# Kernel tuning notes

Hardware: AMD Instinct MI355X
Metric: run time of the kernel (lower is better)

The kernel has to match this reference:

```python
import jax, jax.numpy as jnp
import numpy as np

N, IN_F, E, EDGE_F, H, C = 50000, 128, 800000, 32, 4, 32
NEG_SLOPE = 0.2
EPS = 1e-16


def setup_inputs() -> dict:
    key = jax.random.key(0)
    ks = jax.random.split(key, 10)
    s = lambda *sh: 1.0 / np.sqrt(sh[-1])
    return {
        "node_features": jax.random.normal(ks[0], (N, IN_F), jnp.float32),
        "edge_features": jax.random.normal(ks[1], (E, EDGE_F), jnp.float32),
        "edge_index": jax.random.randint(ks[2], (2, E), 0, N, jnp.int32),
        # GATConv params
        "W_gat": jax.random.normal(ks[3], (H * C, IN_F), jnp.float32) * s(IN_F),
        "att_src": jax.random.normal(ks[4], (H, C), jnp.float32) * s(C),
        "att_dst": jax.random.normal(ks[5], (H, C), jnp.float32) * s(C),
        "att_edge": jax.random.normal(ks[6], (H, C), jnp.float32) * s(C),
        "bias": jnp.zeros((H * C,), jnp.float32),
        # edge_linear and skip_connection weights
        "W_edge": jax.random.normal(ks[7], (H * C, EDGE_F), jnp.float32) * s(EDGE_F),
        "W_skip": jax.random.normal(ks[8], (H * C, IN_F), jnp.float32) * s(IN_F),
    }


def reference(node_features, edge_features, edge_index, W_gat, att_src, att_dst,
              att_edge, bias, W_edge, W_skip):
    src, dst = edge_index[0], edge_index[1]
    # edge_linear + view(-1, H, C)
    e_attr = (edge_features @ W_edge.T).reshape(E, H, C)
    # GATConv: per-head linear transform of nodes -> [N, H, C]
    x = (node_features @ W_gat.T).reshape(N, H, C)
    # attention logits: a_src.x_i + a_dst.x_j + a_edge.e  -> [E, H]
    a_src = jnp.einsum('nhc,hc->nh', x, att_src)
    a_dst = jnp.einsum('nhc,hc->nh', x, att_dst)
    a_edge = jnp.einsum('ehc,hc->eh', e_attr, att_edge)
    alpha = jax.nn.leaky_relu(a_src[src] + a_dst[dst] + a_edge, NEG_SLOPE)
    # segment softmax over incoming edges of each destination node
    m = jax.ops.segment_max(alpha, dst, num_segments=N)  # [N, H]
    m = jnp.where(jnp.isfinite(m), m, 0.0)
    ex = jnp.exp(alpha - m[dst])
    denom = jax.ops.segment_sum(ex, dst, num_segments=N)  # [N, H]
    attn = ex / (denom[dst] + EPS)  # [E, H]
    # message = alpha * x_src ; scatter-add to destination
    msg = x[src] * attn[:, :, None]  # [E, H, C]
    out = jax.ops.segment_sum(msg, dst, num_segments=N)  # [N, H, C]
    out = out.reshape(N, H * C) + bias  # concat=True
    # skip connection + ELU activation
    out = out + node_features @ W_skip.T
    return jax.nn.elu(out)
```

## Files before the change

kernel.cpp:

```cpp
#include <hip/hip_runtime.h>
#include <hip/hip_bf16.h>

constexpr int N_NODES = 50000;
constexpr int IN_F    = 128;
constexpr long E_EDGES = 800000;
constexpr int EDGE_F  = 32;
constexpr int H_HEADS = 4;
constexpr int C_CH    = 32;
constexpr int HC      = 128;
constexpr float NEG_SLOPE = 0.2f;
constexpr float EPS = 1e-16f;
constexpr int NB_SCAN = (N_NODES + 255) / 256;
constexpr int NB_HIST = (int)((E_EDGES + 255) / 256);
constexpr float SM_SHIFT = 12.0f;

typedef __attribute__((ext_vector_type(8))) short bf16x8;
typedef __attribute__((ext_vector_type(4))) float f32x4;

__device__ __forceinline__ unsigned short f2b(float f) {
    __hip_bfloat16 h = __float2bfloat16(f);
    return *reinterpret_cast<unsigned short*>(&h);
}
__device__ __forceinline__ float b2f_lo(unsigned v) { return __uint_as_float(v << 16); }
__device__ __forceinline__ float b2f_hi(unsigned v) { return __uint_as_float(v & 0xffff0000u); }

__global__ __launch_bounds__(256) void zero_counts_kernel(int* __restrict__ counts)
{
    int i = blockIdx.x * 256 + threadIdx.x;
    if (i < N_NODES) counts[i] = 0;
}

__global__ __launch_bounds__(256) void prep_kernel(
    const float* __restrict__ Wg, const float* __restrict__ Ws,
    unsigned short* __restrict__ wcat, const float* __restrict__ We,
    const float* __restrict__ att_edge, float* __restrict__ weff,
    const int* __restrict__ dst, int* __restrict__ counts,
    int* __restrict__ rank)
{
    const int b = blockIdx.x, t = threadIdx.x;
    if (b < 32) {
        int i = (b * 256 + t) * 4;
        const float* srcp = (i < 16384) ? (Wg + i) : (Ws + i - 16384);
        float4 v = *(const float4*)srcp;
        ushort4 o;
        o.x = f2b(v.x); o.y = f2b(v.y); o.z = f2b(v.z); o.w = f2b(v.w);
        *(ushort4*)&wcat[i] = o;
    } else if (b == 32) {
        if (t < 128) {
            int h = t >> 5, f = t & 31;
            float acc = 0.f;
#pragma unroll
            for (int c = 0; c < C_CH; ++c)
                acc = fmaf(We[(h * C_CH + c) * EDGE_F + f], att_edge[h * C_CH + c], acc);
            weff[t] = acc;
        }
    } else {
        long e = (long)(b - 33) * 256 + t;
        if (e < E_EDGES) rank[e] = atomicAdd(&counts[dst[e]], 1);
    }
}

__global__ __launch_bounds__(256) void mfma_gemm_kernel(
    const float* __restrict__ nf, const unsigned short* __restrict__ wcat,
    const float* __restrict__ bias, unsigned short* __restrict__ xb,
    float* __restrict__ out)
{
    const int t  = threadIdx.x;
    const int w  = t >> 6;
    const int l  = t & 63;
    const int lr = l & 15;
    const int lk = l >> 4;
    const int n0 = blockIdx.x * 64;

    bf16x8 bfr[4][4];
#pragma unroll
    for (int nfr = 0; nfr < 4; ++nfr)
#pragma unroll
        for (int ks = 0; ks < 4; ++ks)
            bfr[nfr][ks] = *(const bf16x8*)&wcat[(w * 64 + nfr * 16 + lr) * 128 + ks * 32 + lk * 8];

    f32x4 acc[4][4];
#pragma unroll
    for (int mf = 0; mf < 4; ++mf)
#pragma unroll
        for (int nfr = 0; nfr < 4; ++nfr)
            acc[mf][nfr] = (f32x4){0.f, 0.f, 0.f, 0.f};

#pragma unroll
    for (int ks = 0; ks < 4; ++ks) {
        bf16x8 afr[4];
#pragma unroll
        for (int mf = 0; mf < 4; ++mf) {
            int row = n0 + mf * 16 + lr;
            row = row < N_NODES ? row : N_NODES - 1;
            const float* ap = nf + (size_t)row * IN_F + ks * 32 + lk * 8;
            float4 a0 = *(const float4*)ap;
            float4 a1 = *(const float4*)(ap + 4);
            bf16x8 f;
            f[0] = (short)f2b(a0.x); f[1] = (short)f2b(a0.y);
            f[2] = (short)f2b(a0.z); f[3] = (short)f2b(a0.w);
            f[4] = (short)f2b(a1.x); f[5] = (short)f2b(a1.y);
            f[6] = (short)f2b(a1.z); f[7] = (short)f2b(a1.w);
            afr[mf] = f;
        }
#pragma unroll
        for (int mf = 0; mf < 4; ++mf)
#pragma unroll
            for (int nfr = 0; nfr < 4; ++nfr)
                acc[mf][nfr] = __builtin_amdgcn_mfma_f32_16x16x32_bf16(
                    afr[mf], bfr[nfr][ks], acc[mf][nfr], 0, 0, 0);
    }

#pragma unroll
    for (int nfr = 0; nfr < 4; ++nfr) {
        const int gc = w * 64 + nfr * 16 + lr;
        if (gc < HC) {
#pragma unroll
            for (int mf = 0; mf < 4; ++mf)
#pragma unroll
                for (int r = 0; r < 4; ++r) {
                    int m = n0 + mf * 16 + lk * 4 + r;
                    if (m < N_NODES) xb[(size_t)m * HC + gc] = f2b(acc[mf][nfr][r]);
                }
        } else {
            const float bv = bias[gc - HC];
#pragma unroll
            for (int mf = 0; mf < 4; ++mf)
#pragma unroll
                for (int r = 0; r < 4; ++r) {
                    int m = n0 + mf * 16 + lk * 4 + r;
                    if (m < N_NODES) out[(size_t)m * HC + gc - HC] = acc[mf][nfr][r] + bv;
                }
        }
    }
}

__global__ __launch_bounds__(256) void a_kernel(
    const unsigned int* __restrict__ xb32, const float* __restrict__ att_src,
    const float* __restrict__ att_dst, float* __restrict__ asrc,
    float* __restrict__ adst)
{
    const int wave = threadIdx.x >> 6, lane = threadIdx.x & 63;
    const int n = blockIdx.x * 4 + wave;
    if (n >= N_NODES) return;
    unsigned v = xb32[(size_t)n * 64 + lane];
    float x0 = b2f_lo(v), x1 = b2f_hi(v);
    float2 as = ((const float2*)att_src)[lane];
    float2 ad = ((const float2*)att_dst)[lane];
    float ps = x0 * as.x + x1 * as.y;
    float pd = x0 * ad.x + x1 * ad.y;
#pragma unroll
    for (int off = 1; off < 16; off <<= 1) {
        ps += __shfl_xor(ps, off);
        pd += __shfl_xor(pd, off);
    }
    if ((lane & 15) == 0) {
        asrc[(size_t)n * H_HEADS + (lane >> 4)] = ps;
        adst[(size_t)n * H_HEADS + (lane >> 4)] = pd;
    }
}

__global__ __launch_bounds__(256) void scan1_kernel(const int* __restrict__ counts,
                                                    int* __restrict__ row_ptr,
                                                    int* __restrict__ blocksum)
{
    __shared__ int s[256];
    int t = threadIdx.x;
    int i = blockIdx.x * 256 + t;
    int v = (i < N_NODES) ? counts[i] : 0;
    s[t] = v;
    __syncthreads();
#pragma unroll
    for (int off = 1; off < 256; off <<= 1) {
        int u = (t >= off) ? s[t - off] : 0;
        __syncthreads();
        s[t] += u;
        __syncthreads();
    }
    if (i < N_NODES) row_ptr[i] = s[t] - v;
    if (t == 255) blocksum[blockIdx.x] = s[255];
}

__global__ __launch_bounds__(256) void scan2_kernel(int* __restrict__ blocksum)
{
    __shared__ int s[256];
    int t = threadIdx.x;
    int v = (t < NB_SCAN) ? blocksum[t] : 0;
    s[t] = v;
    __syncthreads();
#pragma unroll
    for (int off = 1; off < 256; off <<= 1) {
        int u = (t >= off) ? s[t - off] : 0;
        __syncthreads();
        s[t] += u;
        __syncthreads();
    }
    blocksum[t] = s[t] - v;
}

__global__ __launch_bounds__(256) void scan3_kernel(int* __restrict__ row_ptr,
                                                    const int* __restrict__ blocksum)
{
    int i = blockIdx.x * 256 + threadIdx.x;
    if (i < N_NODES) row_ptr[i] = row_ptr[i] + blocksum[blockIdx.x];
    if (i == 0) row_ptr[N_NODES] = (int)E_EDGES;
}

__global__ __launch_bounds__(256) void edge_logits_kernel(
    const float* __restrict__ ef, const int* __restrict__ src,
    const int* __restrict__ dst, const float* __restrict__ weff,
    const float* __restrict__ asrc, const float* __restrict__ adst,
    const int* __restrict__ row_ptr, const int* __restrict__ rank,
    unsigned int* __restrict__ rec)
{
    __shared__ float ef_lds[64][36];
    __shared__ float wf[4][36];
    const int t = threadIdx.x;
    const long e0 = (long)blockIdx.x * 64;

#pragma unroll
    for (int j = 0; j < 2; ++j) {
        int i4 = t + j * 256;
        int el = i4 >> 3, f4 = i4 & 7;
        long e = e0 + el;
        float4 v = (e < E_EDGES) ? ((const float4*)ef)[e * 8 + f4]
                                 : make_float4(0.f, 0.f, 0.f, 0.f);
        ef_lds[el][f4 * 4 + 0] = v.x; ef_lds[el][f4 * 4 + 1] = v.y;
        ef_lds[el][f4 * 4 + 2] = v.z; ef_lds[el][f4 * 4 + 3] = v.w;
    }
    if (t < 128) wf[t >> 5][t & 31] = weff[t];
    __syncthreads();

    const int el = t >> 2, h = t & 3;
    const long e = e0 + el;
    if (e < E_EDGES) {
        float acc = 0.f;
#pragma unroll
        for (int f4 = 0; f4 < 8; ++f4) {
            float4 a = *(const float4*)&ef_lds[el][f4 * 4];
            float4 b = *(const float4*)&wf[h][f4 * 4];
            acc = fmaf(a.x, b.x, acc); acc = fmaf(a.y, b.y, acc);
            acc = fmaf(a.z, b.z, acc); acc = fmaf(a.w, b.w, acc);
        }
        int s = src[e], d = dst[e];
        float logit = asrc[(size_t)s * H_HEADS + h] + adst[(size_t)d * H_HEADS + h] + acc;
        float al = logit > 0.f ? logit : NEG_SLOPE * logit;
        int pos = row_ptr[d] + rank[e];
        unsigned w = (__float_as_uint(al) & 0xFFFFFF00u)
                   | ((unsigned)(s >> (8 * h)) & 0xFFu);
        rec[(size_t)pos * 4 + h] = w;
    }
}

__device__ __forceinline__ void accum8(float* acc, uint4 v, float e) {
    acc[0] = fmaf(b2f_lo(v.x), e, acc[0]);
    acc[1] = fmaf(b2f_hi(v.x), e, acc[1]);
    acc[2] = fmaf(b2f_lo(v.y), e, acc[2]);
    acc[3] = fmaf(b2f_hi(v.y), e, acc[3]);
    acc[4] = fmaf(b2f_lo(v.z), e, acc[4]);
    acc[5] = fmaf(b2f_hi(v.z), e, acc[5]);
    acc[6] = fmaf(b2f_lo(v.w), e, acc[6]);
    acc[7] = fmaf(b2f_hi(v.w), e, acc[7]);
}

__device__ __forceinline__ int rec_src(uint4 r) {
    return (int)((r.x & 0xFFu) | ((r.y & 0xFFu) << 8));
}
__device__ __forceinline__ float rec_alpha(uint4 r, int h) {
    unsigned w = h == 0 ? r.x : h == 1 ? r.y : h == 2 ? r.z : r.w;
    return __uint_as_float(w & 0xFFFFFF00u);
}

__global__ __launch_bounds__(256) void aggregate_kernel(
    const int* __restrict__ row_ptr, const uint4* __restrict__ rec4,
    const uint4* __restrict__ xb4, float* __restrict__ out)
{
    const int wave = threadIdx.x >> 6;
    const int lane = threadIdx.x & 63;
    const int d = blockIdx.x * 4 + wave;
    if (d >= N_NODES) return;
    const int beg = row_ptr[d], end = row_ptr[d + 1];
    const int q  = lane >> 4;
    const int cg = lane & 15;
    const int h  = cg >> 2;

    float acc[8] = {0.f, 0.f, 0.f, 0.f, 0.f, 0.f, 0.f, 0.f};
    float dsum = 0.f;

    int i = beg;
    for (; i + 8 <= end; i += 8) {
        int i0 = i + q, i1 = i + 4 + q;
        uint4 r0 = rec4[i0];
        uint4 r1 = rec4[i1];
        int s0 = rec_src(r0);
        int s1 = rec_src(r1);
        float a0 = rec_alpha(r0, h);
        float a1 = rec_alpha(r1, h);
        uint4 v0 = xb4[(size_t)s0 * 16 + cg];
        uint4 v1 = xb4[(size_t)s1 * 16 + cg];
        float e0 = __expf(a0 - SM_SHIFT);
        float e1 = __expf(a1 - SM_SHIFT);
        dsum += e0 + e1;
        accum8(acc, v0, e0);
        accum8(acc, v1, e1);
    }
    for (; i < end; i += 4) {
        int idx = i + q;
        bool val = idx < end;
        int ii = val ? idx : end - 1;
        uint4 r = rec4[ii];
        int s = rec_src(r);
        float a = rec_alpha(r, h);
        uint4 v = xb4[(size_t)s * 16 + cg];
        float e = val ? __expf(a - SM_SHIFT) : 0.f;
        dsum += e;
        accum8(acc, v, e);
    }

#pragma unroll
    for (int off = 16; off <= 32; off <<= 1) {
        dsum += __shfl_xor(dsum, off);
#pragma unroll
        for (int k = 0; k < 8; ++k) acc[k] += __shfl_xor(acc[k], off);
    }
    const float inv = 1.f / (dsum + EPS);

    if (q == 0) {
        float* op = out + (size_t)d * HC + cg * 8;
        float4 o0 = *(const float4*)op;
        float4 o1 = *(const float4*)(op + 4);
        o0.x += acc[0] * inv; o0.y += acc[1] * inv;
        o0.z += acc[2] * inv; o0.w += acc[3] * inv;
        o1.x += acc[4] * inv; o1.y += acc[5] * inv;
        o1.z += acc[6] * inv; o1.w += acc[7] * inv;
        o0.x = o0.x > 0.f ? o0.x : expf(o0.x) - 1.f;
        o0.y = o0.y > 0.f ? o0.y : expf(o0.y) - 1.f;
        o0.z = o0.z > 0.f ? o0.z : expf(o0.z) - 1.f;
        o0.w = o0.w > 0.f ? o0.w : expf(o0.w) - 1.f;
        o1.x = o1.x > 0.f ? o1.x : expf(o1.x) - 1.f;
        o1.y = o1.y > 0.f ? o1.y : expf(o1.y) - 1.f;
        o1.z = o1.z > 0.f ? o1.z : expf(o1.z) - 1.f;
        o1.w = o1.w > 0.f ? o1.w : expf(o1.w) - 1.f;
        *(float4*)op = o0;
        *(float4*)(op + 4) = o1;
    }
}

extern "C" void kernel_launch(void* const* d_in, const int* in_sizes, int n_in,
                              void* d_out, int out_size, void* d_ws, size_t ws_size,
                              hipStream_t stream)
{
    const float* nf       = (const float*)d_in[0];
    const float* ef       = (const float*)d_in[1];
    const int*   ei       = (const int*)d_in[2];
    const float* Wg       = (const float*)d_in[3];
    const float* att_src  = (const float*)d_in[4];
    const float* att_dst  = (const float*)d_in[5];
    const float* att_edge = (const float*)d_in[6];
    const float* bias     = (const float*)d_in[7];
    const float* We       = (const float*)d_in[8];
    const float* Ws       = (const float*)d_in[9];
    float* out = (float*)d_out;

    const int* src = ei;
    const int* dst = ei + E_EDGES;

    unsigned int* rec   = (unsigned int*)d_ws;
    unsigned short* xb  = (unsigned short*)(rec + 4 * E_EDGES);
    unsigned short* wcat= xb + (size_t)N_NODES * HC;
    float* asrc         = (float*)(wcat + 256 * 128);
    float* adst         = asrc + (size_t)N_NODES * H_HEADS;
    float* weff         = adst + (size_t)N_NODES * H_HEADS;
    int*   counts       = (int*)(weff + 128);
    int*   row_ptr      = counts + N_NODES;
    int*   blocksum     = row_ptr + N_NODES + 1;
    int*   rank         = blocksum + 256;

    zero_counts_kernel<<<NB_SCAN, 256, 0, stream>>>(counts);
    prep_kernel<<<33 + NB_HIST, 256, 0, stream>>>(
        Wg, Ws, wcat, We, att_edge, weff, dst, counts, rank);
    mfma_gemm_kernel<<<(N_NODES + 63) / 64, 256, 0, stream>>>(
        nf, wcat, bias, xb, out);
    a_kernel<<<(N_NODES + 3) / 4, 256, 0, stream>>>(
        (const unsigned int*)xb, att_src, att_dst, asrc, adst);
    scan1_kernel<<<NB_SCAN, 256, 0, stream>>>(counts, row_ptr, blocksum);
    scan2_kernel<<<1, 256, 0, stream>>>(blocksum);
    scan3_kernel<<<NB_SCAN, 256, 0, stream>>>(row_ptr, blocksum);
    edge_logits_kernel<<<(int)(E_EDGES / 64), 256, 0, stream>>>(
        ef, src, dst, weff, asrc, adst, row_ptr, rank, rec);
    aggregate_kernel<<<(N_NODES + 3) / 4, 256, 0, stream>>>(
        row_ptr, (const uint4*)rec, (const uint4*)xb, out);
}
```

Baseline: 175.4 us.

## Process one edge per thread in edge logits and batch histogram atomics

The edge logits kernel now gives each thread a whole edge, computing all four heads. Each thread loads the 32 edge features directly as float4s instead of staging them through LDS. It also reads asrc/adst as one float4 each and writes the packed 4-head record as a single uint4, which cuts redundant src/dst/rank/row_ptr loads and scattered 4-byte stores. The histogram part of prep now handles four edges per thread with int4 loads and stores. The risk is more registers per thread and uncoalesced per-thread 128-byte feature reads. The edge logits kernel also drops its bounds check, which relies on E being divisible by 256.

```diff
diff --git a/kernel.cpp b/kernel.cpp
--- a/kernel.cpp
+++ b/kernel.cpp
@@ -11,7 +11,8 @@
 constexpr float NEG_SLOPE = 0.2f;
 constexpr float EPS = 1e-16f;
 constexpr int NB_SCAN = (N_NODES + 255) / 256;
-constexpr int NB_HIST = (int)((E_EDGES + 255) / 256);
+constexpr int NB_EL   = (int)(E_EDGES / 256);
+constexpr int NB_HIST4 = (int)((E_EDGES + 1023) / 1024);
 constexpr float SM_SHIFT = 12.0f;
 
 typedef __attribute__((ext_vector_type(8))) short bf16x8;
@@ -55,8 +56,19 @@
             weff[t] = acc;
         }
     } else {
-        long e = (long)(b - 33) * 256 + t;
-        if (e < E_EDGES) rank[e] = atomicAdd(&counts[dst[e]], 1);
+        long e0 = (long)(b - 33) * 1024 + t * 4;
+        if (e0 + 3 < E_EDGES) {
+            int4 d4 = *(const int4*)(dst + e0);
+            int4 r4;
+            r4.x = atomicAdd(&counts[d4.x], 1);
+            r4.y = atomicAdd(&counts[d4.y], 1);
+            r4.z = atomicAdd(&counts[d4.z], 1);
+            r4.w = atomicAdd(&counts[d4.w], 1);
+            *(int4*)(rank + e0) = r4;
+        } else {
+            for (long e = e0; e < E_EDGES; ++e)
+                rank[e] = atomicAdd(&counts[dst[e]], 1);
+        }
     }
 }
 
@@ -211,45 +223,62 @@
     const int* __restrict__ dst, const float* __restrict__ weff,
     const float* __restrict__ asrc, const float* __restrict__ adst,
     const int* __restrict__ row_ptr, const int* __restrict__ rank,
-    unsigned int* __restrict__ rec)
-{
-    __shared__ float ef_lds[64][36];
-    __shared__ float wf[4][36];
+    uint4* __restrict__ rec4)
+{
+    __shared__ float wf[128];
     const int t = threadIdx.x;
-    const long e0 = (long)blockIdx.x * 64;
-
-#pragma unroll
-    for (int j = 0; j < 2; ++j) {
-        int i4 = t + j * 256;
-        int el = i4 >> 3, f4 = i4 & 7;
-        long e = e0 + el;
-        float4 v = (e < E_EDGES) ? ((const float4*)ef)[e * 8 + f4]
-                                 : make_float4(0.f, 0.f, 0.f, 0.f);
-        ef_lds[el][f4 * 4 + 0] = v.x; ef_lds[el][f4 * 4 + 1] = v.y;
-        ef_lds[el][f4 * 4 + 2] = v.z; ef_lds[el][f4 * 4 + 3] = v.w;
-    }
-    if (t < 128) wf[t >> 5][t & 31] = weff[t];
+    if (t < 128) wf[t] = weff[t];
     __syncthreads();
 
-    const int el = t >> 2, h = t & 3;
-    const long e = e0 + el;
-    if (e < E_EDGES) {
+    const long e = (long)blockIdx.x * 256 + t;
+
+    const int s  = src[e];
+    const int d  = dst[e];
+    const int rk = rank[e];
+    const float4* efp = (const float4*)(ef + (size_t)e * EDGE_F);
+    float4 q0 = efp[0], q1 = efp[1], q2 = efp[2], q3 = efp[3];
+    float4 q4 = efp[4], q5 = efp[5], q6 = efp[6], q7 = efp[7];
+
+    float4 as4 = ((const float4*)asrc)[s];
+    float4 ad4 = ((const float4*)adst)[d];
+    const int pos = row_ptr[d] + rk;
+
+    uint4 r;
+    unsigned* rw = (unsigned*)&r;
+    float base[4] = {as4.x + ad4.x, as4.y + ad4.y, as4.z + ad4.z, as4.w + ad4.w};
+#pragma unroll
+    for (int h = 0; h < 4; ++h) {
+        const float4 w0 = *(const float4*)&wf[h * 32 + 0];
+        const float4 w1 = *(const float4*)&wf[h * 32 + 4];
+        const float4 w2 = *(const float4*)&wf[h * 32 + 8];
+        const float4 w3 = *(const float4*)&wf[h * 32 + 12];
+        const float4 w4 = *(const float4*)&wf[h * 32 + 16];
+        const float4 w5 = *(const float4*)&wf[h * 32 + 20];
+        const float4 w6 = *(const float4*)&wf[h * 32 + 24];
+        const float4 w7 = *(const float4*)&wf[h * 32 + 28];
         float acc = 0.f;
-#pragma unroll
-        for (int f4 = 0; f4 < 8; ++f4) {
-            float4 a = *(const float4*)&ef_lds[el][f4 * 4];
-            float4 b = *(const float4*)&wf[h][f4 * 4];
-            acc = fmaf(a.x, b.x, acc); acc = fmaf(a.y, b.y, acc);
-            acc = fmaf(a.z, b.z, acc); acc = fmaf(a.w, b.w, acc);
-        }
-        int s = src[e], d = dst[e];
-        float logit = asrc[(size_t)s * H_HEADS + h] + adst[(size_t)d * H_HEADS + h] + acc;
+        acc = fmaf(q0.x, w0.x, acc); acc = fmaf(q0.y, w0.y, acc);
+        acc = fmaf(q0.z, w0.z, acc); acc = fmaf(q0.w, w0.w, acc);
+        acc = fmaf(q1.x, w1.x, acc); acc = fmaf(q1.y, w1.y, acc);
+        acc = fmaf(q1.z, w1.z, acc); acc = fmaf(q1.w, w1.w, acc);
+        acc = fmaf(q2.x, w2.x, acc); acc = fmaf(q2.y, w2.y, acc);
+        acc = fmaf(q2.z, w2.z, acc); acc = fmaf(q2.w, w2.w, acc);
+        acc = fmaf(q3.x, w3.x, acc); acc = fmaf(q3.y, w3.y, acc);
+        acc = fmaf(q3.z, w3.z, acc); acc = fmaf(q3.w, w3.w, acc);
+        acc = fmaf(q4.x, w4.x, acc); acc = fmaf(q4.y, w4.y, acc);
+        acc = fmaf(q4.z, w4.z, acc); acc = fmaf(q4.w, w4.w, acc);
+        acc = fmaf(q5.x, w5.x, acc); acc = fmaf(q5.y, w5.y, acc);
+        acc = fmaf(q5.z, w5.z, acc); acc = fmaf(q5.w, w5.w, acc);
+        acc = fmaf(q6.x, w6.x, acc); acc = fmaf(q6.y, w6.y, acc);
+        acc = fmaf(q6.z, w6.z, acc); acc = fmaf(q6.w, w6.w, acc);
+        acc = fmaf(q7.x, w7.x, acc); acc = fmaf(q7.y, w7.y, acc);
+        acc = fmaf(q7.z, w7.z, acc); acc = fmaf(q7.w, w7.w, acc);
+        float logit = base[h] + acc;
         float al = logit > 0.f ? logit : NEG_SLOPE * logit;
-        int pos = row_ptr[d] + rank[e];
-        unsigned w = (__float_as_uint(al) & 0xFFFFFF00u)
-                   | ((unsigned)(s >> (8 * h)) & 0xFFu);
-        rec[(size_t)pos * 4 + h] = w;
-    }
+        rw[h] = (__float_as_uint(al) & 0xFFFFFF00u)
+              | ((unsigned)(s >> (8 * h)) & 0xFFu);
+    }
+    rec4[pos] = r;
 }
 
 __device__ __forceinline__ void accum8(float* acc, uint4 v, float e) {
@@ -377,7 +406,7 @@
     int*   rank         = blocksum + 256;
 
     zero_counts_kernel<<<NB_SCAN, 256, 0, stream>>>(counts);
-    prep_kernel<<<33 + NB_HIST, 256, 0, stream>>>(
+    prep_kernel<<<33 + NB_HIST4, 256, 0, stream>>>(
         Wg, Ws, wcat, We, att_edge, weff, dst, counts, rank);
     mfma_gemm_kernel<<<(N_NODES + 63) / 64, 256, 0, stream>>>(
         nf, wcat, bias, xb, out);
@@ -386,8 +415,8 @@
     scan1_kernel<<<NB_SCAN, 256, 0, stream>>>(counts, row_ptr, blocksum);
     scan2_kernel<<<1, 256, 0, stream>>>(blocksum);
     scan3_kernel<<<NB_SCAN, 256, 0, stream>>>(row_ptr, blocksum);
-    edge_logits_kernel<<<(int)(E_EDGES / 64), 256, 0, stream>>>(
-        ef, src, dst, weff, asrc, adst, row_ptr, rank, rec);
+    edge_logits_kernel<<<NB_EL, 256, 0, stream>>>(
+        ef, src, dst, weff, asrc, adst, row_ptr, rank, (uint4*)rec);
     aggregate_kernel<<<(N_NODES + 3) / 4, 256, 0, stream>>>(
         row_ptr, (const uint4*)rec, (const uint4*)xb, out);
 }
```

Result: slower. 191.1 us (+8.9%).

## Precompute edge logits in histogram kernel and vectorize edge record scatter

Applied to the files above, without the earlier changes.

The per-edge edge-feature dot product against the folded attention weights moves into a new prep kernel. That kernel runs alongside the vectorized atomic histogram (four edges per thread) and writes a float4 per edge to a new workspace buffer. The edge_logits kernel now uses one thread per edge, reads float4 asrc/adst/ae, and writes one uint4 record to its CSR slot instead of four scalar scattered writes. Zeroing the counts is merged into the setup kernel, which removes one launch. In exchange the edge features take an extra 12.8MB round trip through the ae buffer.

```diff
diff --git a/kernel.cpp b/kernel.cpp
--- a/kernel.cpp
+++ b/kernel.cpp
@@ -11,7 +11,9 @@
 constexpr float NEG_SLOPE = 0.2f;
 constexpr float EPS = 1e-16f;
 constexpr int NB_SCAN = (N_NODES + 255) / 256;
-constexpr int NB_HIST = (int)((E_EDGES + 255) / 256);
+constexpr int NB_EL   = (int)(E_EDGES / 256);
+constexpr int NB_HIST4 = (int)((E_EDGES + 1023) / 1024);
+constexpr int NB_AE   = (int)(E_EDGES / 64);
 constexpr float SM_SHIFT = 12.0f;
 
 typedef __attribute__((ext_vector_type(8))) short bf16x8;
@@ -24,18 +26,11 @@
 __device__ __forceinline__ float b2f_lo(unsigned v) { return __uint_as_float(v << 16); }
 __device__ __forceinline__ float b2f_hi(unsigned v) { return __uint_as_float(v & 0xffff0000u); }
 
-__global__ __launch_bounds__(256) void zero_counts_kernel(int* __restrict__ counts)
-{
-    int i = blockIdx.x * 256 + threadIdx.x;
-    if (i < N_NODES) counts[i] = 0;
-}
-
-__global__ __launch_bounds__(256) void prep_kernel(
+__global__ __launch_bounds__(256) void setup_kernel(
     const float* __restrict__ Wg, const float* __restrict__ Ws,
     unsigned short* __restrict__ wcat, const float* __restrict__ We,
     const float* __restrict__ att_edge, float* __restrict__ weff,
-    const int* __restrict__ dst, int* __restrict__ counts,
-    int* __restrict__ rank)
+    int* __restrict__ counts)
 {
     const int b = blockIdx.x, t = threadIdx.x;
     if (b < 32) {
@@ -55,9 +50,59 @@
             weff[t] = acc;
         }
     } else {
-        long e = (long)(b - 33) * 256 + t;
-        if (e < E_EDGES) rank[e] = atomicAdd(&counts[dst[e]], 1);
-    }
+        int i = (b - 33) * 256 + t;
+        if (i < N_NODES) counts[i] = 0;
+    }
+}
+
+__global__ __launch_bounds__(256) void prep2_kernel(
+    const int* __restrict__ dst, int* __restrict__ counts,
+    int* __restrict__ rank, const float* __restrict__ ef,
+    const float* __restrict__ weff, float* __restrict__ ae)
+{
+    const int b = blockIdx.x, t = threadIdx.x;
+    if (b < NB_HIST4) {
+        long e0 = (long)b * 1024 + t * 4;
+        if (e0 + 3 < E_EDGES) {
+            int4 d4 = *(const int4*)(dst + e0);
+            int4 r4;
+            r4.x = atomicAdd(&counts[d4.x], 1);
+            r4.y = atomicAdd(&counts[d4.y], 1);
+            r4.z = atomicAdd(&counts[d4.z], 1);
+            r4.w = atomicAdd(&counts[d4.w], 1);
+            *(int4*)(rank + e0) = r4;
+        } else {
+            for (long e = e0; e < E_EDGES; ++e)
+                rank[e] = atomicAdd(&counts[dst[e]], 1);
+        }
+        return;
+    }
+
+    __shared__ float ef_lds[64][36];
+    __shared__ float wf[4][36];
+    const long e0 = (long)(b - NB_HIST4) * 64;
+
+#pragma unroll
+    for (int j = 0; j < 2; ++j) {
+        int i4 = t + j * 256;
+        int el = i4 >> 3, f4 = i4 & 7;
+        float4 v = ((const float4*)ef)[(e0 + el) * 8 + f4];
+        ef_lds[el][f4 * 4 + 0] = v.x; ef_lds[el][f4 * 4 + 1] = v.y;
+        ef_lds[el][f4 * 4 + 2] = v.z; ef_lds[el][f4 * 4 + 3] = v.w;
+    }
+    if (t < 128) wf[t >> 5][t & 31] = weff[t];
+    __syncthreads();
+
+    const int el = t >> 2, h = t & 3;
+    float acc = 0.f;
+#pragma unroll
+    for (int f4 = 0; f4 < 8; ++f4) {
+        float4 a = *(const float4*)&ef_lds[el][f4 * 4];
+        float4 w = *(const float4*)&wf[h][f4 * 4];
+        acc = fmaf(a.x, w.x, acc); acc = fmaf(a.y, w.y, acc);
+        acc = fmaf(a.z, w.z, acc); acc = fmaf(a.w, w.w, acc);
+    }
+    ae[e0 * 4 + t] = acc;
 }
 
 __global__ __launch_bounds__(256) void mfma_gemm_kernel(
@@ -207,49 +252,33 @@
 }
 
 __global__ __launch_bounds__(256) void edge_logits_kernel(
-    const float* __restrict__ ef, const int* __restrict__ src,
-    const int* __restrict__ dst, const float* __restrict__ weff,
-    const float* __restrict__ asrc, const float* __restrict__ adst,
-    const int* __restrict__ row_ptr, const int* __restrict__ rank,
-    unsigned int* __restrict__ rec)
-{
-    __shared__ float ef_lds[64][36];
-    __shared__ float wf[4][36];
-    const int t = threadIdx.x;
-    const long e0 = (long)blockIdx.x * 64;
-
-#pragma unroll
-    for (int j = 0; j < 2; ++j) {
-        int i4 = t + j * 256;
-        int el = i4 >> 3, f4 = i4 & 7;
-        long e = e0 + el;
-        float4 v = (e < E_EDGES) ? ((const float4*)ef)[e * 8 + f4]
-                                 : make_float4(0.f, 0.f, 0.f, 0.f);
-        ef_lds[el][f4 * 4 + 0] = v.x; ef_lds[el][f4 * 4 + 1] = v.y;
-        ef_lds[el][f4 * 4 + 2] = v.z; ef_lds[el][f4 * 4 + 3] = v.w;
-    }
-    if (t < 128) wf[t >> 5][t & 31] = weff[t];
-    __syncthreads();
-
-    const int el = t >> 2, h = t & 3;
-    const long e = e0 + el;
-    if (e < E_EDGES) {
-        float acc = 0.f;
-#pragma unroll
-        for (int f4 = 0; f4 < 8; ++f4) {
-            float4 a = *(const float4*)&ef_lds[el][f4 * 4];
-            float4 b = *(const float4*)&wf[h][f4 * 4];
-            acc = fmaf(a.x, b.x, acc); acc = fmaf(a.y, b.y, acc);
-            acc = fmaf(a.z, b.z, acc); acc = fmaf(a.w, b.w, acc);
-        }
-        int s = src[e], d = dst[e];
-        float logit = asrc[(size_t)s * H_HEADS + h] + adst[(size_t)d * H_HEADS + h] + acc;
-        float al = logit > 0.f ? logit : NEG_SLOPE * logit;
-        int pos = row_ptr[d] + rank[e];
-        unsigned w = (__float_as_uint(al) & 0xFFFFFF00u)
-                   | ((unsigned)(s >> (8 * h)) & 0xFFu);
-        rec[(size_t)pos * 4 + h] = w;
-    }
+    const int* __restrict__ src, const int* __restrict__ dst,
+    const float* __restrict__ ae, const float* __restrict__ asrc,
+    const float* __restrict__ adst, const int* __restrict__ row_ptr,
+    const int* __restrict__ rank, uint4* __restrict__ rec4)
+{
+    const long e = (long)blockIdx.x * 256 + threadIdx.x;
+
+    const int s  = src[e];
+    const int d  = dst[e];
+    const int rk = rank[e];
+    float4 a_e = ((const float4*)ae)[e];
+
+    float4 as4 = ((const float4*)asrc)[s];
+    float4 ad4 = ((const float4*)adst)[d];
+    const int pos = row_ptr[d] + rk;
+
+    float lg[4] = {as4.x + ad4.x + a_e.x, as4.y + ad4.y + a_e.y,
+                   as4.z + ad4.z + a_e.z, as4.w + ad4.w + a_e.w};
+    uint4 r;
+    unsigned* rw = (unsigned*)&r;
+#pragma unroll
+    for (int h = 0; h < 4; ++h) {
+        float al = lg[h] > 0.f ? lg[h] : NEG_SLOPE * lg[h];
+        rw[h] = (__float_as_uint(al) & 0xFFFFFF00u)
+              | ((unsigned)(s >> (8 * h)) & 0xFFu);
+    }
+    rec4[pos] = r;
 }
 
 __device__ __forceinline__ void accum8(float* acc, uint4 v, float e) {
@@ -366,7 +395,8 @@
     const int* dst = ei + E_EDGES;
 
     unsigned int* rec   = (unsigned int*)d_ws;
-    unsigned short* xb  = (unsigned short*)(rec + 4 * E_EDGES);
+    float* ae           = (float*)(rec + 4 * E_EDGES);
+    unsigned short* xb  = (unsigned short*)(ae + 4 * E_EDGES);
     unsigned short* wcat= xb + (size_t)N_NODES * HC;
     float* asrc         = (float*)(wcat + 256 * 128);
     float* adst         = asrc + (size_t)N_NODES * H_HEADS;
@@ -376,9 +406,10 @@
     int*   blocksum     = row_ptr + N_NODES + 1;
     int*   rank         = blocksum + 256;
 
-    zero_counts_kernel<<<NB_SCAN, 256, 0, stream>>>(counts);
-    prep_kernel<<<33 + NB_HIST, 256, 0, stream>>>(
-        Wg, Ws, wcat, We, att_edge, weff, dst, counts, rank);
+    setup_kernel<<<33 + NB_SCAN, 256, 0, stream>>>(
+        Wg, Ws, wcat, We, att_edge, weff, counts);
+    prep2_kernel<<<NB_HIST4 + NB_AE, 256, 0, stream>>>(
+        dst, counts, rank, ef, weff, ae);
     mfma_gemm_kernel<<<(N_NODES + 63) / 64, 256, 0, stream>>>(
         nf, wcat, bias, xb, out);
     a_kernel<<<(N_NODES + 3) / 4, 256, 0, stream>>>(
@@ -386,8 +417,8 @@
     scan1_kernel<<<NB_SCAN, 256, 0, stream>>>(counts, row_ptr, blocksum);
     scan2_kernel<<<1, 256, 0, stream>>>(blocksum);
     scan3_kernel<<<NB_SCAN, 256, 0, stream>>>(row_ptr, blocksum);
-    edge_logits_kernel<<<(int)(E_EDGES / 64), 256, 0, stream>>>(
-        ef, src, dst, weff, asrc, adst, row_ptr, rank, rec);
+    edge_logits_kernel<<<NB_EL, 256, 0, stream>>>(
+        src, dst, ae, asrc, adst, row_ptr, rank, (uint4*)rec);
     aggregate_kernel<<<(N_NODES + 3) / 4, 256, 0, stream>>>(
         row_ptr, (const uint4*)rec, (const uint4*)xb, out);
 }
```

Result: no change. 176.6 us (+0.7%).
